# Performance work log

Hardware: AMD Instinct MI355X
Metric: run time of the kernel (lower is better)

The kernel has to match this reference:

```python
import jax, jax.numpy as jnp
import numpy as np
import math

PI = math.pi
L = 6.0 * math.pi
EPS = 1e-5


def c19_activation(x, rho=4.0):
    scaled = x * (1.0 / PI)
    n = jnp.floor(scaled)
    t = scaled - n
    h = t * (1.0 - t)
    sgn = jnp.where(jnp.remainder(n, 2.0) < 1.0, 1.0, -1.0)
    core = PI * (sgn * h + rho * h * h)
    return jnp.where(x >= L, x - L, jnp.where(x <= -L, x + L, core))


def layer_norm(x, gamma, beta):
    mu = jnp.mean(x, axis=-1, keepdims=True)
    var = jnp.mean(jnp.square(x - mu), axis=-1, keepdims=True)
    return (x - mu) * jax.lax.rsqrt(var + EPS) * gamma + beta


def setup_inputs() -> dict:
    key = jax.random.key(0)
    ks = jax.random.split(key, 8)
    B, T, NB, D, DEPTH = 65536, 32, 8, 128, 4
    nl = DEPTH - 1  # 3 inner layers
    x = jax.random.normal(ks[0], (B, T, NB), dtype=jnp.float32)
    Wi = jax.random.normal(ks[1], (NB, D), dtype=jnp.float32) * 0.1   # input_proj (in, out)
    bi = jnp.zeros((D,), jnp.float32)
    Wo = jax.random.normal(ks[2], (D, NB), dtype=jnp.float32) * 0.1   # output_proj
    bo = jnp.zeros((NB,), jnp.float32)
    g_state = jnp.ones((D,), jnp.float32)
    b_state = jnp.zeros((D,), jnp.float32)
    Ws = jax.random.normal(ks[3], (nl, D, D), dtype=jnp.float32) * (1.0 / math.sqrt(D))
    bs = jnp.zeros((nl, D), jnp.float32)
    gs = jnp.ones((nl, D), jnp.float32)
    betas = jnp.zeros((nl, D), jnp.float32)
    return {"x": x, "Wi": Wi, "bi": bi, "Wo": Wo, "bo": bo,
            "g_state": g_state, "b_state": b_state,
            "Ws": Ws, "bs": bs, "gs": gs, "betas": betas}


def reference(x, Wi, bi, Wo, bo, g_state, b_state, Ws, bs, gs, betas):
    B, T, _ = x.shape
    D = Wi.shape[1]
    nl = Ws.shape[0]

    def step(h, xt):  # h: [B,D], xt: [B,NB]
        inp = xt @ Wi + bi
        state = 0.618 * layer_norm(h, g_state, b_state) + 0.382 * inp
        for i in range(nl):  # fixed small depth loop
            state = state + c19_activation(layer_norm(state, gs[i], betas[i]) @ Ws[i] + bs[i])
        out = state @ Wo + bo
        return state, out

    h0 = jnp.zeros((B, D), dtype=x.dtype)
    _, outs = jax.lax.scan(step, h0, jnp.swapaxes(x, 0, 1))  # outs: [T,B,NB]
    return jnp.swapaxes(outs, 0, 1)  # [B,T,NB]
```

## Files before the change

kernel.cpp:

```cpp
#include <hip/hip_runtime.h>
#include <math.h>

#define BDIM 1024
#define BR   64
#define D    128
#define SPD  130
#define SWOP 12
#define TT   32
#define NB   8
#define NL   3

typedef double v4d __attribute__((ext_vector_type(4)));

__device__ __forceinline__ double c19_act_d(double x) {
    const double PI_D = 3.14159265358979323846;
    const double L6   = 6.0 * PI_D;
    double scaled = x * (1.0 / PI_D);
    double n = floor(scaled);
    double t = scaled - n;
    double h = t * (1.0 - t);
    double halfn = n * 0.5;
    double fr = halfn - floor(halfn);
    double sgn = (fr < 0.25) ? 1.0 : -1.0;
    double core = PI_D * (sgn * h + 4.0 * h * h);
    double r = core;
    r = (x <= -L6) ? (x + L6) : r;
    r = (x >=  L6) ? (x - L6) : r;
    return r;
}

__global__ void miniphi_prep(const float* __restrict__ Ws, const float* __restrict__ gs,
                             double* __restrict__ wp) {
    int idx = blockIdx.x * 256 + threadIdx.x;
    wp[idx] = (double)gs[idx >> 7] * (double)Ws[idx];
}

__global__ __launch_bounds__(BDIM) void miniphi_kernel(
    const float* __restrict__ x,  const float* __restrict__ Wi, const float* __restrict__ bi,
    const float* __restrict__ Wo, const float* __restrict__ bo,
    const float* __restrict__ g_state, const float* __restrict__ b_state,
    const float* __restrict__ Ws, const float* __restrict__ bs,
    const float* __restrict__ gs, const float* __restrict__ betas,
    const double* __restrict__ wp,
    float* __restrict__ out)
{
    __shared__ double sState[BR][SPD];
    __shared__ float  sWi[NB][D];
    __shared__ float  sWo[D][SWOP];
    __shared__ float  sBi[D], sGst[D], sBst[D];
    __shared__ double sGW[NL][D];
    __shared__ double sBWbs[NL][D];
    __shared__ double sRstd[BR], sMu2[BR];
    __shared__ float  sBo[NB];
    __shared__ int    sPR[64][4], sPC[64][4];
    __shared__ int    sFlag;

    const int tid  = threadIdx.x;
    const int lane = tid & 63;
    const int wv   = tid >> 6;

    for (int i = tid; i < NB * D; i += BDIM) sWi[i >> 7][i & 127] = Wi[i];
    for (int i = tid; i < D * NB; i += BDIM) sWo[i >> 3][i & 7] = Wo[i];
    for (int i = tid; i < D; i += BDIM) { sBi[i] = bi[i]; sGst[i] = g_state[i]; sBst[i] = b_state[i]; }
    if (tid < NB) sBo[tid] = bo[tid];
    for (int i = tid; i < BR * D; i += BDIM) sState[i >> 7][i & 127] = 0.0;
    if (tid < NL * D) {
        int ly = tid >> 7, c = tid & 127;
        const float* wl = Ws + (size_t)ly * D * D;
        double gw = 0.0, bw = 0.0;
        for (int k = 0; k < D; ++k) {
            double w = (double)wl[k * D + c];
            gw = fma((double)gs[ly * D + k], w, gw);
            bw = fma((double)betas[ly * D + k], w, bw);
        }
        sGW[ly][c] = gw;
        sBWbs[ly][c] = bw + (double)bs[ly * D + c];
    }

    if (wv == 0) {
        const int plm = lane & 15, plk = lane >> 4;
        v4d z = {0.0, 0.0, 0.0, 0.0};
        v4d p1 = __builtin_amdgcn_mfma_f64_16x16x4f64((double)plm, 1.0, z, 0, 0, 0);
        v4d p2 = __builtin_amdgcn_mfma_f64_16x16x4f64(1.0, (double)plm, z, 0, 0, 0);
        double pk = (double)(1 << plk);
        v4d p3 = __builtin_amdgcn_mfma_f64_16x16x4f64(pk, pk, z, 0, 0, 0);
        v4d p4 = __builtin_amdgcn_mfma_f64_16x16x4f64(1.0 + 0x1p-30, 1.0, z, 0, 0, 0);
        double pa5 = (plk == 0) ? 1.0 : 0x1p-52;
        v4d p5 = __builtin_amdgcn_mfma_f64_16x16x4f64(pa5, 1.0, z, 0, 0, 0);
        bool ok = true;
        #pragma unroll
        for (int i = 0; i < 4; ++i) {
            double v = p1[i]; int r = (int)(v * 0.25 + 0.5);
            ok = ok && (v == 4.0 * (double)r) && (r >= 0) && (r < 16);
            sPR[lane][i] = r;
            double w = p2[i]; int c2 = (int)(w * 0.25 + 0.5);
            ok = ok && (w == 4.0 * (double)c2) && (c2 >= 0) && (c2 < 16);
            sPC[lane][i] = c2;
            ok = ok && (p3[i] == 85.0);
            ok = ok && (p4[i] == 4.0 + 0x1p-28);
            ok = ok && (p5[i] == 1.0 + 3.0 * 0x1p-52);
        }
        unsigned long long bal = __ballot(ok ? 1 : 0);
        if (lane == 0) sFlag = (bal == 0xFFFFFFFFFFFFFFFFull) ? 1 : 0;
    }
    __syncthreads();
    const int useMfma = sFlag && (wp != nullptr);

    const int rLN = tid >> 4;
    const int sL  = tid & 15;
    const int lm  = lane & 15, lk = lane >> 4;
    const int rb  = (wv >> 3) * 32;
    const int c0  = (wv & 7) * 16;
    const int r0v = wv * 4;
    const size_t rowg = (size_t)blockIdx.x * BR;

    #define LN_BLOCK                                                                \
      { double sum = 0.0;                                                           \
        _Pragma("unroll")                                                           \
        for (int j = 0; j < 8; ++j) sum += sState[rLN][sL + 16 * j];                \
        sum += __shfl_xor(sum, 1); sum += __shfl_xor(sum, 2);                       \
        sum += __shfl_xor(sum, 4); sum += __shfl_xor(sum, 8);                       \
        double mu = sum * (1.0 / 128.0);                                            \
        double sq = 0.0;                                                            \
        _Pragma("unroll")                                                           \
        for (int j = 0; j < 8; ++j) { double dd = sState[rLN][sL + 16 * j] - mu; sq += dd * dd; } \
        sq += __shfl_xor(sq, 1); sq += __shfl_xor(sq, 2);                           \
        sq += __shfl_xor(sq, 4); sq += __shfl_xor(sq, 8);                           \
        double rstd = 1.0 / sqrt(sq * (1.0 / 128.0) + 1e-5);                        \
        if (sL == 0) { sRstd[rLN] = rstd; sMu2[rLN] = mu * rstd; } }

    #define MFMA_QR(QK)                                                             \
      { double b_[8];                                                               \
        _Pragma("unroll")                                                           \
        for (int i_ = 0; i_ < 8; ++i_)                                              \
            b_[i_] = bsrc[(size_t)((QK) + i_ * 4 + lk) * D];                        \
        _Pragma("unroll")                                                           \
        for (int i_ = 0; i_ < 8; ++i_) {                                            \
            double a0 = sState[rb + lm     ][(QK) + i_ * 4 + lk];                   \
            double a1 = sState[rb + lm + 16][(QK) + i_ * 4 + lk];                   \
            acc0 = __builtin_amdgcn_mfma_f64_16x16x4f64(a0, b_[i_], acc0, 0, 0, 0); \
            acc1 = __builtin_amdgcn_mfma_f64_16x16x4f64(a1, b_[i_], acc1, 0, 0, 0); \
        } }

    for (int t = 0; t < TT; ++t) {
        {
            const float* xp = x + (rowg + (size_t)rLN) * (TT * NB) + (size_t)t * NB;
            float4 xa = *(const float4*)(xp);
            float4 xb = *(const float4*)(xp + 4);
            float xf[8] = {xa.x, xa.y, xa.z, xa.w, xb.x, xb.y, xb.z, xb.w};

            double sum = 0.0;
            #pragma unroll
            for (int j = 0; j < 8; ++j) sum += sState[rLN][sL + 16 * j];
            sum += __shfl_xor(sum, 1); sum += __shfl_xor(sum, 2);
            sum += __shfl_xor(sum, 4); sum += __shfl_xor(sum, 8);
            double mu = sum * (1.0 / 128.0);
            double sq = 0.0;
            #pragma unroll
            for (int j = 0; j < 8; ++j) { double dd = sState[rLN][sL + 16 * j] - mu; sq += dd * dd; }
            sq += __shfl_xor(sq, 1); sq += __shfl_xor(sq, 2);
            sq += __shfl_xor(sq, 4); sq += __shfl_xor(sq, 8);
            double rstd = 1.0 / sqrt(sq * (1.0 / 128.0) + 1e-5);

            #pragma unroll
            for (int j = 0; j < 8; ++j) {
                int c = sL + 16 * j;
                double v = sState[rLN][c];
                double inp = (double)sBi[c];
                #pragma unroll
                for (int k = 0; k < 8; ++k)
                    inp = fma((double)xf[k], (double)sWi[k][c], inp);
                double ln = (v - mu) * rstd * (double)sGst[c] + (double)sBst[c];
                sState[rLN][c] = 0.618 * ln + 0.382 * inp;
            }
        }
        __syncthreads();

        for (int ly = 0; ly < NL; ++ly) {
            if (useMfma) {
                v4d acc0 = {0,0,0,0}, acc1 = {0,0,0,0};
                const double* bsrc = wp + (size_t)ly * D * D + c0 + lm;
                MFMA_QR(0)
                MFMA_QR(32)
                MFMA_QR(64)
                MFMA_QR(96)
                LN_BLOCK
                __syncthreads();
                #pragma unroll
                for (int i = 0; i < 4; ++i) {
                    int col = c0 + sPC[lane][i];
                    int R0  = rb + sPR[lane][i];
                    double gwc = sGW[ly][col], bwc = sBWbs[ly][col];
                    double y0 = fma(sRstd[R0],      acc0[i], fma(-sMu2[R0],      gwc, bwc));
                    double y1 = fma(sRstd[R0 + 16], acc1[i], fma(-sMu2[R0 + 16], gwc, bwc));
                    sState[R0][col]      += c19_act_d(y0);
                    sState[R0 + 16][col] += c19_act_d(y1);
                }
            } else {
                double acc0[4] = {0,0,0,0}, acc1[4] = {0,0,0,0};
                const size_t lyb = (size_t)ly * D * D;
                #pragma unroll 4
                for (int kg = 0; kg < D; kg += 2) {
                    double b00, b01, b10, b11;
                    if (wp) {
                        b00 = wp[lyb + (size_t)kg * D + lane];
                        b01 = wp[lyb + (size_t)kg * D + lane + 64];
                        b10 = wp[lyb + (size_t)(kg + 1) * D + lane];
                        b11 = wp[lyb + (size_t)(kg + 1) * D + lane + 64];
                    } else {
                        double g0 = (double)gs[ly * D + kg], g1 = (double)gs[ly * D + kg + 1];
                        b00 = g0 * (double)Ws[lyb + (size_t)kg * D + lane];
                        b01 = g0 * (double)Ws[lyb + (size_t)kg * D + lane + 64];
                        b10 = g1 * (double)Ws[lyb + (size_t)(kg + 1) * D + lane];
                        b11 = g1 * (double)Ws[lyb + (size_t)(kg + 1) * D + lane + 64];
                    }
                    #pragma unroll
                    for (int r = 0; r < 4; ++r) {
                        double2 a = *(const double2*)&sState[r0v + r][kg];
                        acc0[r] = fma(a.y, b10, fma(a.x, b00, acc0[r]));
                        acc1[r] = fma(a.y, b11, fma(a.x, b01, acc1[r]));
                    }
                }
                LN_BLOCK
                __syncthreads();
                double gwc0 = sGW[ly][lane],   gwc1 = sGW[ly][lane + 64];
                double bwc0 = sBWbs[ly][lane], bwc1 = sBWbs[ly][lane + 64];
                #pragma unroll
                for (int r = 0; r < 4; ++r) {
                    int R = r0v + r;
                    double rs = sRstd[R], m2 = sMu2[R];
                    double y0 = fma(rs, acc0[r], fma(-m2, gwc0, bwc0));
                    double y1 = fma(rs, acc1[r], fma(-m2, gwc1, bwc1));
                    sState[R][lane]      += c19_act_d(y0);
                    sState[R][lane + 64] += c19_act_d(y1);
                }
            }
            __syncthreads();
        }

        #pragma unroll
        for (int p = 0; p < 2; ++p) {
            double accj[4] = {0.0, 0.0, 0.0, 0.0};
            #pragma unroll
            for (int u = 0; u < 8; ++u) {
                int k = sL + 16 * u;
                double s = sState[rLN][k];
                float4 w = *(const float4*)&sWo[k][4 * p];
                accj[0] = fma(s, (double)w.x, accj[0]);
                accj[1] = fma(s, (double)w.y, accj[1]);
                accj[2] = fma(s, (double)w.z, accj[2]);
                accj[3] = fma(s, (double)w.w, accj[3]);
            }
            #pragma unroll
            for (int j = 0; j < 4; ++j) {
                accj[j] += __shfl_xor(accj[j], 1);
                accj[j] += __shfl_xor(accj[j], 2);
                accj[j] += __shfl_xor(accj[j], 4);
                accj[j] += __shfl_xor(accj[j], 8);
            }
            int jloc = sL - 4 * p;
            double o = accj[0];
            #pragma unroll
            for (int j = 1; j < 4; ++j) o = (jloc == j) ? accj[j] : o;
            if (jloc >= 0 && jloc < 4)
                out[((rowg + (size_t)rLN) * TT + (size_t)t) * NB + sL] =
                    (float)(o + (double)sBo[sL]);
        }
    }
    #undef MFMA_QR
    #undef LN_BLOCK
}

extern "C" void kernel_launch(void* const* d_in, const int* in_sizes, int n_in,
                              void* d_out, int out_size, void* d_ws, size_t ws_size,
                              hipStream_t stream) {
    const float* x       = (const float*)d_in[0];
    const float* Wi      = (const float*)d_in[1];
    const float* bi      = (const float*)d_in[2];
    const float* Wo      = (const float*)d_in[3];
    const float* bo      = (const float*)d_in[4];
    const float* g_state = (const float*)d_in[5];
    const float* b_state = (const float*)d_in[6];
    const float* Ws      = (const float*)d_in[7];
    const float* bs      = (const float*)d_in[8];
    const float* gs      = (const float*)d_in[9];
    const float* betas   = (const float*)d_in[10];
    float* out = (float*)d_out;

    const size_t wp_bytes = (size_t)NL * D * D * sizeof(double);
    double* wp = (ws_size >= wp_bytes) ? (double*)d_ws : nullptr;
    if (wp) {
        dim3 pgrid(NL * D * D / 256), pblock(256);
        hipLaunchKernelGGL(miniphi_prep, pgrid, pblock, 0, stream, Ws, gs, wp);
    }

    const int B = in_sizes[0] / (TT * NB);
    dim3 grid(B / BR), block(BDIM);
    hipLaunchKernelGGL(miniphi_kernel, grid, block, 0, stream,
                       x, Wi, bi, Wo, bo, g_state, b_state, Ws, bs, gs, betas, wp, out);
}
```

Measured before the change: 5.065 ms.

## Software-pipeline MFMA GEMM and activation epilogue across two row halves

```diff
diff --git a/kernel.cpp b/kernel.cpp
--- a/kernel.cpp
+++ b/kernel.cpp
@@ -106,16 +106,17 @@
     __syncthreads();
     const int useMfma = sFlag && (wp != nullptr);
 
-    const int rLN = tid >> 4;
-    const int sL  = tid & 15;
-    const int lm  = lane & 15, lk = lane >> 4;
-    const int rb  = (wv >> 3) * 32;
-    const int c0  = (wv & 7) * 16;
-    const int r0v = wv * 4;
+    const int rLN  = tid >> 4;
+    const int sL   = tid & 15;
+    const int lm   = lane & 15, lk = lane >> 4;
+    const int rt16 = (wv >> 3) * 16;
+    const int c0   = (wv & 7) * 16;
+    const int r0v  = wv * 4;
     const size_t rowg = (size_t)blockIdx.x * BR;
 
-    #define LN_BLOCK                                                                \
-      { double sum = 0.0;                                                           \
+    #define LN_HALF(HB)                                                             \
+      if ((rLN & 32) == (HB)) {                                                     \
+        double sum = 0.0;                                                           \
         _Pragma("unroll")                                                           \
         for (int j = 0; j < 8; ++j) sum += sState[rLN][sL + 16 * j];                \
         sum += __shfl_xor(sum, 1); sum += __shfl_xor(sum, 2);                       \
@@ -129,17 +130,29 @@
         double rstd = 1.0 / sqrt(sq * (1.0 / 128.0) + 1e-5);                        \
         if (sL == 0) { sRstd[rLN] = rstd; sMu2[rLN] = mu * rstd; } }
 
-    #define MFMA_QR(QK)                                                             \
-      { double b_[8];                                                               \
+    #define G_HALF(ACC, HB, LY)                                                     \
+      { const double* bsrc = wp + (size_t)(LY) * D * D + c0 + lm;                   \
         _Pragma("unroll")                                                           \
-        for (int i_ = 0; i_ < 8; ++i_)                                              \
-            b_[i_] = bsrc[(size_t)((QK) + i_ * 4 + lk) * D];                        \
-        _Pragma("unroll")                                                           \
-        for (int i_ = 0; i_ < 8; ++i_) {                                            \
-            double a0 = sState[rb + lm     ][(QK) + i_ * 4 + lk];                   \
-            double a1 = sState[rb + lm + 16][(QK) + i_ * 4 + lk];                   \
-            acc0 = __builtin_amdgcn_mfma_f64_16x16x4f64(a0, b_[i_], acc0, 0, 0, 0); \
-            acc1 = __builtin_amdgcn_mfma_f64_16x16x4f64(a1, b_[i_], acc1, 0, 0, 0); \
+        for (int q_ = 0; q_ < 4; ++q_) {                                            \
+            double b_[8];                                                           \
+            _Pragma("unroll")                                                       \
+            for (int i_ = 0; i_ < 8; ++i_)                                          \
+                b_[i_] = bsrc[(size_t)(q_ * 32 + i_ * 4 + lk) * D];                 \
+            _Pragma("unroll")                                                       \
+            for (int i_ = 0; i_ < 8; ++i_) {                                        \
+                double a_ = sState[(HB) + rt16 + lm][q_ * 32 + i_ * 4 + lk];        \
+                ACC = __builtin_amdgcn_mfma_f64_16x16x4f64(a_, b_[i_], ACC, 0, 0, 0); \
+            }                                                                       \
+        } }
+
+    #define E_HALF(ACC, HB, LY)                                                     \
+      { _Pragma("unroll")                                                           \
+        for (int i_ = 0; i_ < 4; ++i_) {                                            \
+            int col = c0 + sPC[lane][i_];                                           \
+            int R0  = (HB) + rt16 + sPR[lane][i_];                                  \
+            double gwc = sGW[LY][col], bwc = sBWbs[LY][col];                        \
+            double y_ = fma(sRstd[R0], ACC[i_], fma(-sMu2[R0], gwc, bwc));          \
+            sState[R0][col] += c19_act_d(y_);                                       \
         } }
 
     for (int t = 0; t < TT; ++t) {
@@ -176,27 +189,29 @@
         }
         __syncthreads();
 
-        for (int ly = 0; ly < NL; ++ly) {
-            if (useMfma) {
-                v4d acc0 = {0,0,0,0}, acc1 = {0,0,0,0};
-                const double* bsrc = wp + (size_t)ly * D * D + c0 + lm;
-                MFMA_QR(0)
-                MFMA_QR(32)
-                MFMA_QR(64)
-                MFMA_QR(96)
-                LN_BLOCK
-                __syncthreads();
-                #pragma unroll
-                for (int i = 0; i < 4; ++i) {
-                    int col = c0 + sPC[lane][i];
-                    int R0  = rb + sPR[lane][i];
-                    double gwc = sGW[ly][col], bwc = sBWbs[ly][col];
-                    double y0 = fma(sRstd[R0],      acc0[i], fma(-sMu2[R0],      gwc, bwc));
-                    double y1 = fma(sRstd[R0 + 16], acc1[i], fma(-sMu2[R0 + 16], gwc, bwc));
-                    sState[R0][col]      += c19_act_d(y0);
-                    sState[R0 + 16][col] += c19_act_d(y1);
-                }
-            } else {
+        if (useMfma) {
+            v4d accA = {0,0,0,0}, accB = {0,0,0,0};
+            G_HALF(accA, 0, 0)  LN_HALF(0)
+            __syncthreads();
+            accB = (v4d){0,0,0,0};
+            G_HALF(accB, 32, 0) LN_HALF(32) E_HALF(accA, 0, 0)
+            __syncthreads();
+            accA = (v4d){0,0,0,0};
+            G_HALF(accA, 0, 1)  LN_HALF(0)  E_HALF(accB, 32, 0)
+            __syncthreads();
+            accB = (v4d){0,0,0,0};
+            G_HALF(accB, 32, 1) LN_HALF(32) E_HALF(accA, 0, 1)
+            __syncthreads();
+            accA = (v4d){0,0,0,0};
+            G_HALF(accA, 0, 2)  LN_HALF(0)  E_HALF(accB, 32, 1)
+            __syncthreads();
+            accB = (v4d){0,0,0,0};
+            G_HALF(accB, 32, 2) LN_HALF(32) E_HALF(accA, 0, 2)
+            __syncthreads();
+            E_HALF(accB, 32, 2)
+            __syncthreads();
+        } else {
+            for (int ly = 0; ly < NL; ++ly) {
                 double acc0[4] = {0,0,0,0}, acc1[4] = {0,0,0,0};
                 const size_t lyb = (size_t)ly * D * D;
                 #pragma unroll 4
@@ -221,7 +236,7 @@
                         acc1[r] = fma(a.y, b11, fma(a.x, b01, acc1[r]));
                     }
                 }
-                LN_BLOCK
+                LN_HALF(0) LN_HALF(32)
                 __syncthreads();
                 double gwc0 = sGW[ly][lane],   gwc1 = sGW[ly][lane + 64];
                 double bwc0 = sBWbs[ly][lane], bwc1 = sBWbs[ly][lane + 64];
@@ -234,8 +249,8 @@
                     sState[R][lane]      += c19_act_d(y0);
                     sState[R][lane + 64] += c19_act_d(y1);
                 }
+                __syncthreads();
             }
-            __syncthreads();
         }
 
         #pragma unroll
@@ -267,8 +282,9 @@
                     (float)(o + (double)sBo[sL]);
         }
     }
-    #undef MFMA_QR
-    #undef LN_BLOCK
+    #undef E_HALF
+    #undef G_HALF
+    #undef LN_HALF
 }
 
 extern "C" void kernel_launch(void* const* d_in, const int* in_sizes, int n_in,
```

After: 11.64 ms. 2.3x slower.
